# Kernel tuning notes

Hardware: AMD Instinct MI355X
Metric: run time of the kernel (lower is better)

## Reference

```python
import jax, jax.numpy as jnp
import numpy as np

N_NODES = 50000
N_EDGES = 800000
IN_DIM = 256
HID_DIM = 512
OUT_DIM = 256


def setup_inputs() -> dict:
    key = jax.random.key(0)
    ks = jax.random.split(key, 8)
    x = jax.random.normal(ks[0], (N_NODES, IN_DIM), dtype=jnp.float32)
    src = jax.random.randint(ks[1], (N_EDGES,), 0, N_NODES, dtype=jnp.int32)
    dst = jax.random.randint(ks[2], (N_EDGES,), 0, N_NODES, dtype=jnp.int32)
    s = 1.0 / np.sqrt(IN_DIM)
    W_self = jax.random.uniform(ks[3], (IN_DIM, HID_DIM), jnp.float32, -s, s)
    W_neigh = jax.random.uniform(ks[4], (IN_DIM, HID_DIM), jnp.float32, -s, s)
    b_enc = jnp.zeros((HID_DIM,), jnp.float32)
    s2 = 1.0 / np.sqrt(HID_DIM)
    W_dec = jax.random.uniform(ks[5], (HID_DIM, OUT_DIM), jnp.float32, -s2, s2)
    b_dec = jax.random.uniform(ks[6], (OUT_DIM,), jnp.float32, -s2, s2)
    return {"x": x, "src": src, "dst": dst, "W_self": W_self,
            "W_neigh": W_neigh, "b_enc": b_enc, "W_dec": W_dec, "b_dec": b_dec}


def reference(x, src, dst, W_self, W_neigh, b_enc, W_dec, b_dec):
    n = x.shape[0]
    # mean neighbor aggregation: scatter-sum src features onto dst, divide by in-degree
    deg = jax.ops.segment_sum(jnp.ones(dst.shape, x.dtype), dst, num_segments=n)
    neigh_sum = jax.ops.segment_sum(x[src], dst, num_segments=n)  # [N, in_dim]
    neigh_mean = neigh_sum / jnp.clip(deg, 1.0)[:, None]
    # SAGEConv 'mean': fc_self(x) + fc_neigh(h_neigh) + bias, then relu
    h = jax.nn.relu(x @ W_self + neigh_mean @ W_neigh + b_enc)  # [N, hid]
    reconstructed = h @ W_dec + b_dec  # [N, out]
    return (reconstructed, h)
```

## Files before the change

### kernel.cpp

```cpp
#include <hip/hip_runtime.h>
#include <stdint.h>

#define N_NODES 50000
#define N_EDGES 800000
#define IN_DIM 256
#define HID_DIM 512
#define OUT_DIM 256
#define SCAN_BLOCKS 196

__device__ __forceinline__ uint16_t f2b(float f) {
    uint32_t u = __builtin_bit_cast(uint32_t, f);
    uint32_t r = (u + 0x7fffu + ((u >> 16) & 1u)) >> 16;
    return (uint16_t)r;
}
__device__ __forceinline__ float b2f(uint16_t h) {
    uint32_t u = ((uint32_t)h) << 16;
    return __builtin_bit_cast(float, u);
}

__device__ __forceinline__ void async_copy16(const void* g, void* l) {
    __builtin_amdgcn_global_load_lds(
        (const __attribute__((address_space(1))) uint32_t*)g,
        (__attribute__((address_space(3))) uint32_t*)l,
        16, 0, 0);
}

typedef __bf16 bf16x8 __attribute__((ext_vector_type(8)));
typedef float f32x4 __attribute__((ext_vector_type(4)));

#if __has_builtin(__builtin_amdgcn_cvt_pk_fp8_f32) && __has_builtin(__builtin_amdgcn_cvt_pk_f32_fp8)
#define HW_FP8 1
#endif

__device__ __forceinline__ uint8_t enc_e4m3_sw(float f) {
    uint32_t u = __builtin_bit_cast(uint32_t, f);
    uint32_t s = (u >> 24) & 0x80u;
    float a = fabsf(f);
    if (!(a > 0.f)) return (uint8_t)s;
    if (a >= 448.f) return (uint8_t)(s | 0x7E);
    int ebits = (int)((u >> 23) & 255u) - 127;
    if (ebits < -6) {
        int q = (int)rintf(a * 512.0f);
        if (q <= 0) return (uint8_t)s;
        if (q < 8)  return (uint8_t)(s | (uint32_t)q);
        return (uint8_t)(s | 0x08u);
    }
    float scale = exp2f((float)(3 - ebits));
    int q = (int)rintf(a * scale);
    if (q == 16) { ebits++; q = 8; }
    return (uint8_t)(s | (uint32_t)((ebits + 7) << 3) | (uint32_t)(q - 8));
}
__device__ __forceinline__ float dec_e4m3_sw(uint32_t b) {
    uint32_t sgn = b >> 7, e = (b >> 3) & 15u, m = b & 7u;
    float v;
    if (e) v = __builtin_bit_cast(float, ((e + 120u) << 23) | (m << 20));
    else   v = (float)m * 0.001953125f;
    return sgn ? -v : v;
}

__device__ __forceinline__ uint32_t pack4_fp8(float4 v) {
#ifdef HW_FP8
    int w = 0;
    w = __builtin_amdgcn_cvt_pk_fp8_f32(v.x, v.y, w, false);
    w = __builtin_amdgcn_cvt_pk_fp8_f32(v.z, v.w, w, true);
    return (uint32_t)w;
#else
    return (uint32_t)enc_e4m3_sw(v.x) | ((uint32_t)enc_e4m3_sw(v.y) << 8) |
           ((uint32_t)enc_e4m3_sw(v.z) << 16) | ((uint32_t)enc_e4m3_sw(v.w) << 24);
#endif
}
__device__ __forceinline__ void unpack4_fp8(uint32_t w, float f[4]) {
#ifdef HW_FP8
    auto lo = __builtin_amdgcn_cvt_pk_f32_fp8((int)w, false);
    auto hi = __builtin_amdgcn_cvt_pk_f32_fp8((int)w, true);
    f[0] = lo[0]; f[1] = lo[1]; f[2] = hi[0]; f[3] = hi[1];
#else
    f[0] = dec_e4m3_sw(w & 255u); f[1] = dec_e4m3_sw((w >> 8) & 255u);
    f[2] = dec_e4m3_sw((w >> 16) & 255u); f[3] = dec_e4m3_sw(w >> 24);
#endif
}

__global__ void k_prep(const float* __restrict__ x, uint16_t* __restrict__ A,
                       uint32_t* __restrict__ Xq,
                       const float* __restrict__ Ws, const float* __restrict__ Wn,
                       const float* __restrict__ Wd,
                       uint16_t* __restrict__ Wc, uint16_t* __restrict__ Wt,
                       uint32_t* __restrict__ deg) {
    int b = blockIdx.x, t = threadIdx.x;
    if (b < 12500) {
        int id = b * 256 + t;
        int row = id >> 6, q = id & 63;
        float4 v = ((const float4*)x)[id];
        ushort4 o;
        o.x = f2b(v.x); o.y = f2b(v.y); o.z = f2b(v.z); o.w = f2b(v.w);
        *(ushort4*)(A + (size_t)row * 512 + q * 4) = o;
        Xq[id] = pack4_fp8(v);
    } else if (b < 12696) {
        int i = (b - 12500) * 256 + t;
        if (i < N_NODES) deg[i] = 0u;
    } else if (b < 13720) {
        int id = (b - 12696) * 256 + t;
        int n = id >> 9, k = id & 511;
        float v = (k < 256) ? Ws[(size_t)k * 512 + n] : Wn[(size_t)(k - 256) * 512 + n];
        Wc[(size_t)n * 512 + k] = f2b(v);
    } else {
        int id = (b - 13720) * 256 + t;
        int n = id >> 9, k = id & 511;
        Wt[(size_t)n * 512 + k] = f2b(Wd[(size_t)k * 256 + n]);
    }
}

__global__ void k_deg(const int* __restrict__ dst, uint32_t* __restrict__ deg) {
    int e = blockIdx.x * 256 + threadIdx.x;
    if (e < N_EDGES) atomicAdd(&deg[dst[e]], 1u);
}

__global__ void k_scan1(const uint32_t* __restrict__ deg, uint32_t* __restrict__ psum) {
    __shared__ uint32_t wsum[4];
    int b = blockIdx.x, t = threadIdx.x;
    int i = b * 256 + t;
    int v = (i < N_NODES) ? (int)deg[i] : 0;
#pragma unroll
    for (int o = 1; o < 64; o <<= 1) v += __shfl_xor(v, o);
    if ((t & 63) == 0) wsum[t >> 6] = (uint32_t)v;
    __syncthreads();
    if (t == 0) psum[b] = wsum[0] + wsum[1] + wsum[2] + wsum[3];
}

__global__ void k_scan2(const uint32_t* __restrict__ psum, uint32_t* __restrict__ pbase,
                        uint32_t* __restrict__ off) {
    __shared__ uint32_t sb[256];
    int t = threadIdx.x;
    uint32_t v = (t < SCAN_BLOCKS) ? psum[t] : 0u;
    sb[t] = v;
    __syncthreads();
#pragma unroll
    for (int o = 1; o < 256; o <<= 1) {
        uint32_t u = (t >= o) ? sb[t - o] : 0u;
        __syncthreads();
        sb[t] += u;
        __syncthreads();
    }
    if (t < SCAN_BLOCKS) pbase[t] = sb[t] - v;
    if (t == 0) off[N_NODES] = N_EDGES;
}

__global__ void k_scan3(const uint32_t* __restrict__ deg, const uint32_t* __restrict__ pbase,
                        uint32_t* __restrict__ off, uint32_t* __restrict__ cur) {
    __shared__ uint32_t sb[256];
    int b = blockIdx.x, t = threadIdx.x;
    int i = b * 256 + t;
    uint32_t v = (i < N_NODES) ? deg[i] : 0u;
    sb[t] = v;
    __syncthreads();
#pragma unroll
    for (int o = 1; o < 256; o <<= 1) {
        uint32_t u = (t >= o) ? sb[t - o] : 0u;
        __syncthreads();
        sb[t] += u;
        __syncthreads();
    }
    if (i < N_NODES) {
        uint32_t e = pbase[b] + sb[t] - v;
        off[i] = e;
        cur[i] = e;
    }
}

__global__ void k_scatter(const int* __restrict__ src, const int* __restrict__ dst,
                          uint32_t* __restrict__ cur, int* __restrict__ esrc) {
    int e = blockIdx.x * 256 + threadIdx.x;
    if (e >= N_EDGES) return;
    int d = dst[e];
    uint32_t pos = atomicAdd(&cur[d], 1u);
    esrc[pos] = src[e];
}

__global__ __launch_bounds__(256) void k_agg(const uint32_t* __restrict__ off,
                                             const int* __restrict__ esrc,
                                             const uint32_t* __restrict__ Xq,
                                             uint16_t* __restrict__ A) {
    int node = blockIdx.x * 4 + (threadIdx.x >> 6);
    if (node >= N_NODES) return;
    int lane = threadIdx.x & 63;
    const uint32_t* Xl = Xq + lane;
    uint32_t s0 = off[node], s1 = off[node + 1];
    float a0 = 0.f, a1 = 0.f, a2 = 0.f, a3 = 0.f;
    uint32_t j = s0;
    for (; j + 8 <= s1; j += 8) {
        int s_[8];
#pragma unroll
        for (int t = 0; t < 8; ++t) s_[t] = esrc[j + t];
        uint32_t w_[8];
#pragma unroll
        for (int t = 0; t < 8; ++t) w_[t] = Xl[(size_t)s_[t] * 64];
#pragma unroll
        for (int t = 0; t < 8; ++t) {
            float f[4];
            unpack4_fp8(w_[t], f);
            a0 += f[0]; a1 += f[1]; a2 += f[2]; a3 += f[3];
        }
    }
    if (j + 4 <= s1) {
        int s_[4];
#pragma unroll
        for (int t = 0; t < 4; ++t) s_[t] = esrc[j + t];
        uint32_t w_[4];
#pragma unroll
        for (int t = 0; t < 4; ++t) w_[t] = Xl[(size_t)s_[t] * 64];
#pragma unroll
        for (int t = 0; t < 4; ++t) {
            float f[4];
            unpack4_fp8(w_[t], f);
            a0 += f[0]; a1 += f[1]; a2 += f[2]; a3 += f[3];
        }
        j += 4;
    }
    for (; j < s1; ++j) {
        uint32_t w0 = Xl[(size_t)esrc[j] * 64];
        float f[4];
        unpack4_fp8(w0, f);
        a0 += f[0]; a1 += f[1]; a2 += f[2]; a3 += f[3];
    }
    float inv = 1.0f / (float)max(s1 - s0, 1u);
    ushort4 o;
    o.x = f2b(a0 * inv); o.y = f2b(a1 * inv); o.z = f2b(a2 * inv); o.w = f2b(a3 * inv);
    *(ushort4*)(A + (size_t)node * 512 + 256 + lane * 4) = o;
}

template <int N, int NY, bool RELU, bool WBF16>
__global__ __launch_bounds__(256, 2) void k_gemm(const uint16_t* __restrict__ A,
                                                 const uint16_t* __restrict__ Bt,
                                                 const float* __restrict__ bias,
                                                 float* __restrict__ Cf,
                                                 uint16_t* __restrict__ Cb, int M) {
    constexpr int K = 512;
    constexpr int BK = 64;
    __shared__ __align__(1024) uint16_t As[128 * BK];
    __shared__ __align__(1024) uint16_t Bs[128 * BK];
    const int tid = threadIdx.x;
    const int wave = tid >> 6, lane = tid & 63;
    const int wm = wave >> 1, wn = wave & 1;

    const int nwg = gridDim.x;
    const int bid = blockIdx.x;
    const int xcd = bid & 7, o = bid >> 3;
    const int q = nwg >> 3, r = nwg & 7;
    const int work = (xcd < r ? xcd * (q + 1) : r * (q + 1) + (xcd - r) * q) + o;
    const int m0 = (work / NY) * 128;
    const int n0 = (work % NY) * 128;

    const int l15 = lane & 15, l4 = lane >> 4;

    f32x4 acc[4][4] = {};

    for (int k0 = 0; k0 < K; k0 += BK) {
        __syncthreads();
#pragma unroll
        for (int j = 0; j < 4; ++j) {
            int c = j * 256 + tid;
            int row = c >> 3, p = c & 7;
            int s = p ^ (row & 7);
            int grA = min(m0 + row, M - 1);
            async_copy16(A + (size_t)grA * 512 + k0 + s * 8,
                         (char*)As + j * 4096 + wave * 1024);
            int grB = n0 + row;
            async_copy16(Bt + (size_t)grB * 512 + k0 + s * 8,
                         (char*)Bs + j * 4096 + wave * 1024);
        }
        __syncthreads();
#pragma unroll
        for (int kk = 0; kk < 2; ++kk) {
            bf16x8 af[4], bfr[4];
#pragma unroll
            for (int m = 0; m < 4; ++m) {
                int row = wm * 64 + m * 16 + l15;
                int s = (kk * 4 + l4) ^ (row & 7);
                af[m] = *(const bf16x8*)((const char*)As + row * 128 + s * 16);
            }
#pragma unroll
            for (int n = 0; n < 4; ++n) {
                int row = wn * 64 + n * 16 + l15;
                int s = (kk * 4 + l4) ^ (row & 7);
                bfr[n] = *(const bf16x8*)((const char*)Bs + row * 128 + s * 16);
            }
#pragma unroll
            for (int m = 0; m < 4; ++m)
#pragma unroll
                for (int n = 0; n < 4; ++n)
                    acc[m][n] = __builtin_amdgcn_mfma_f32_16x16x32_bf16(
                        af[m], bfr[n], acc[m][n], 0, 0, 0);
        }
    }

#pragma unroll
    for (int m = 0; m < 4; ++m) {
        int rbase = m0 + wm * 64 + m * 16 + l4 * 4;
#pragma unroll
        for (int i = 0; i < 4; ++i) {
            int r2 = rbase + i;
            if (r2 < M) {
#pragma unroll
                for (int n = 0; n < 4; ++n) {
                    int cidx = n0 + wn * 64 + n * 16 + l15;
                    float v = acc[m][n][i] + bias[cidx];
                    if (RELU) v = fmaxf(v, 0.f);
                    Cf[(size_t)r2 * N + cidx] = v;
                    if constexpr (WBF16) Cb[(size_t)r2 * N + cidx] = f2b(v);
                }
            }
        }
    }
}

extern "C" void kernel_launch(void* const* d_in, const int* in_sizes, int n_in,
                              void* d_out, int out_size, void* d_ws, size_t ws_size,
                              hipStream_t stream) {
    const float* x     = (const float*)d_in[0];
    const int*   src   = (const int*)d_in[1];
    const int*   dst   = (const int*)d_in[2];
    const float* Wself = (const float*)d_in[3];
    const float* Wneigh= (const float*)d_in[4];
    const float* benc  = (const float*)d_in[5];
    const float* Wdec  = (const float*)d_in[6];
    const float* bdec  = (const float*)d_in[7];

    float* out_recon = (float*)d_out;
    float* out_h     = (float*)d_out + (size_t)N_NODES * OUT_DIM;

    char* ws = (char*)d_ws;
    uint16_t* A    = (uint16_t*)(ws);
    uint16_t* Hb   = (uint16_t*)(ws + 51200000);
    uint16_t* Wc   = (uint16_t*)(ws + 102400000);
    uint16_t* Wd   = (uint16_t*)(ws + 102924288);
    uint32_t* deg  = (uint32_t*)(ws + 103186432);
    uint32_t* off  = (uint32_t*)(ws + 103386432);
    uint32_t* cur  = (uint32_t*)(ws + 103586560);
    int*     esrc  = (int*)(ws + 103786560);
    uint32_t* psum = (uint32_t*)(ws + 106986560);
    uint32_t* pbase= (uint32_t*)(ws + 106987344);
    uint32_t* Xq   = (uint32_t*)(ws + 106988544);

    k_prep<<<14232, 256, 0, stream>>>(x, A, Xq, Wself, Wneigh, Wdec, Wc, Wd, deg);
    k_deg<<<3125, 256, 0, stream>>>(dst, deg);
    k_scan1<<<SCAN_BLOCKS, 256, 0, stream>>>(deg, psum);
    k_scan2<<<1, 256, 0, stream>>>(psum, pbase, off);
    k_scan3<<<SCAN_BLOCKS, 256, 0, stream>>>(deg, pbase, off, cur);
    k_scatter<<<3125, 256, 0, stream>>>(src, dst, cur, esrc);
    k_agg<<<12500, 256, 0, stream>>>(off, esrc, Xq, A);
    k_gemm<512, 4, true, true><<<1564, 256, 0, stream>>>(A, Wc, benc, out_h, Hb, N_NODES);
    k_gemm<256, 2, false, false><<<782, 256, 0, stream>>>(Hb, Wd, bdec, out_recon, nullptr, N_NODES);
}
```

Baseline: 226.5 us.

## Drop bf16 H copy; decoder reads fp32 H and converts in-kernel; merge scan kernels

The encoder GEMM no longer writes a separate bf16 copy of h. The decoder GEMM now loads the fp32 h output directly and converts it to bf16 while staging it into LDS. This removes a 51 MB write, but the decoder must read twice the bytes with synchronous loads instead of async LDS copies. Separately, the two scan phases are fused: each block computes its own base by reducing the preceding partial sums, which removes one kernel launch.

```diff
diff --git a/kernel.cpp b/kernel.cpp
--- a/kernel.cpp
+++ b/kernel.cpp
@@ -127,32 +127,20 @@
     if (t == 0) psum[b] = wsum[0] + wsum[1] + wsum[2] + wsum[3];
 }
 
-__global__ void k_scan2(const uint32_t* __restrict__ psum, uint32_t* __restrict__ pbase,
-                        uint32_t* __restrict__ off) {
+__global__ void k_scan23(const uint32_t* __restrict__ deg, const uint32_t* __restrict__ psum,
+                         uint32_t* __restrict__ off, uint32_t* __restrict__ cur) {
     __shared__ uint32_t sb[256];
-    int t = threadIdx.x;
-    uint32_t v = (t < SCAN_BLOCKS) ? psum[t] : 0u;
-    sb[t] = v;
-    __syncthreads();
-#pragma unroll
-    for (int o = 1; o < 256; o <<= 1) {
-        uint32_t u = (t >= o) ? sb[t - o] : 0u;
-        __syncthreads();
-        sb[t] += u;
-        __syncthreads();
-    }
-    if (t < SCAN_BLOCKS) pbase[t] = sb[t] - v;
-    if (t == 0) off[N_NODES] = N_EDGES;
-}
-
-__global__ void k_scan3(const uint32_t* __restrict__ deg, const uint32_t* __restrict__ pbase,
-                        uint32_t* __restrict__ off, uint32_t* __restrict__ cur) {
-    __shared__ uint32_t sb[256];
+    __shared__ uint32_t wsum[4];
     int b = blockIdx.x, t = threadIdx.x;
     int i = b * 256 + t;
+    uint32_t pv = (t < b) ? psum[t] : 0u;
+#pragma unroll
+    for (int o = 1; o < 64; o <<= 1) pv += __shfl_xor(pv, o);
+    if ((t & 63) == 0) wsum[t >> 6] = pv;
     uint32_t v = (i < N_NODES) ? deg[i] : 0u;
     sb[t] = v;
     __syncthreads();
+    uint32_t base = wsum[0] + wsum[1] + wsum[2] + wsum[3];
 #pragma unroll
     for (int o = 1; o < 256; o <<= 1) {
         uint32_t u = (t >= o) ? sb[t - o] : 0u;
@@ -161,10 +149,11 @@
         __syncthreads();
     }
     if (i < N_NODES) {
-        uint32_t e = pbase[b] + sb[t] - v;
+        uint32_t e = base + sb[t] - v;
         off[i] = e;
         cur[i] = e;
     }
+    if (b == 0 && t == 0) off[N_NODES] = N_EDGES;
 }
 
 __global__ void k_scatter(const int* __restrict__ src, const int* __restrict__ dst,
@@ -228,12 +217,11 @@
     *(ushort4*)(A + (size_t)node * 512 + 256 + lane * 4) = o;
 }
 
-template <int N, int NY, bool RELU, bool WBF16>
-__global__ __launch_bounds__(256, 2) void k_gemm(const uint16_t* __restrict__ A,
-                                                 const uint16_t* __restrict__ Bt,
-                                                 const float* __restrict__ bias,
-                                                 float* __restrict__ Cf,
-                                                 uint16_t* __restrict__ Cb, int M) {
+template <int N, int NY, bool RELU>
+__global__ __launch_bounds__(256, 2) void k_gemm_enc(const uint16_t* __restrict__ A,
+                                                     const uint16_t* __restrict__ Bt,
+                                                     const float* __restrict__ bias,
+                                                     float* __restrict__ Cf, int M) {
     constexpr int K = 512;
     constexpr int BK = 64;
     __shared__ __align__(1024) uint16_t As[128 * BK];
@@ -306,7 +294,98 @@
                     float v = acc[m][n][i] + bias[cidx];
                     if (RELU) v = fmaxf(v, 0.f);
                     Cf[(size_t)r2 * N + cidx] = v;
-                    if constexpr (WBF16) Cb[(size_t)r2 * N + cidx] = f2b(v);
+                }
+            }
+        }
+    }
+}
+
+template <int N, int NY>
+__global__ __launch_bounds__(256, 2) void k_gemm_dec(const float* __restrict__ Af,
+                                                     const uint16_t* __restrict__ Bt,
+                                                     const float* __restrict__ bias,
+                                                     float* __restrict__ Cf, int M) {
+    constexpr int K = 512;
+    constexpr int BK = 64;
+    __shared__ __align__(1024) uint16_t As[128 * BK];
+    __shared__ __align__(1024) uint16_t Bs[128 * BK];
+    const int tid = threadIdx.x;
+    const int wave = tid >> 6, lane = tid & 63;
+    const int wm = wave >> 1, wn = wave & 1;
+
+    const int nwg = gridDim.x;
+    const int bid = blockIdx.x;
+    const int xcd = bid & 7, o = bid >> 3;
+    const int q = nwg >> 3, r = nwg & 7;
+    const int work = (xcd < r ? xcd * (q + 1) : r * (q + 1) + (xcd - r) * q) + o;
+    const int m0 = (work / NY) * 128;
+    const int n0 = (work % NY) * 128;
+
+    const int l15 = lane & 15, l4 = lane >> 4;
+
+    f32x4 acc[4][4] = {};
+
+    for (int k0 = 0; k0 < K; k0 += BK) {
+        __syncthreads();
+#pragma unroll
+        for (int j = 0; j < 4; ++j) {
+            int c = j * 256 + tid;
+            int row = c >> 3, p = c & 7;
+            int grB = n0 + row;
+            async_copy16(Bt + (size_t)grB * 512 + k0 + (p ^ (row & 7)) * 8,
+                         (char*)Bs + j * 4096 + wave * 1024);
+        }
+#pragma unroll
+        for (int j = 0; j < 4; ++j) {
+            int c = j * 256 + tid;
+            int row = c >> 3, p = c & 7;
+            int grA = min(m0 + row, M - 1);
+            const float* srcp = Af + (size_t)grA * 512 + k0 + p * 8;
+            float4 v0 = *(const float4*)(srcp);
+            float4 v1 = *(const float4*)(srcp + 4);
+            uint32_t d0 = (uint32_t)f2b(v0.x) | ((uint32_t)f2b(v0.y) << 16);
+            uint32_t d1 = (uint32_t)f2b(v0.z) | ((uint32_t)f2b(v0.w) << 16);
+            uint32_t d2 = (uint32_t)f2b(v1.x) | ((uint32_t)f2b(v1.y) << 16);
+            uint32_t d3 = (uint32_t)f2b(v1.z) | ((uint32_t)f2b(v1.w) << 16);
+            *(uint4*)((char*)As + row * 128 + (p ^ (row & 7)) * 16) =
+                make_uint4(d0, d1, d2, d3);
+        }
+        __syncthreads();
+#pragma unroll
+        for (int kk = 0; kk < 2; ++kk) {
+            bf16x8 af[4], bfr[4];
+#pragma unroll
+            for (int m = 0; m < 4; ++m) {
+                int row = wm * 64 + m * 16 + l15;
+                int s = (kk * 4 + l4) ^ (row & 7);
+                af[m] = *(const bf16x8*)((const char*)As + row * 128 + s * 16);
+            }
+#pragma unroll
+            for (int n = 0; n < 4; ++n) {
+                int row = wn * 64 + n * 16 + l15;
+                int s = (kk * 4 + l4) ^ (row & 7);
+                bfr[n] = *(const bf16x8*)((const char*)Bs + row * 128 + s * 16);
+            }
+#pragma unroll
+            for (int m = 0; m < 4; ++m)
+#pragma unroll
+                for (int n = 0; n < 4; ++n)
+                    acc[m][n] = __builtin_amdgcn_mfma_f32_16x16x32_bf16(
+                        af[m], bfr[n], acc[m][n], 0, 0, 0);
+        }
+    }
+
+#pragma unroll
+    for (int m = 0; m < 4; ++m) {
+        int rbase = m0 + wm * 64 + m * 16 + l4 * 4;
+#pragma unroll
+        for (int i = 0; i < 4; ++i) {
+            int r2 = rbase + i;
+            if (r2 < M) {
+#pragma unroll
+                for (int n = 0; n < 4; ++n) {
+                    int cidx = n0 + wn * 64 + n * 16 + l15;
+                    Cf[(size_t)r2 * N + cidx] = acc[m][n][i] + bias[cidx];
                 }
             }
         }
@@ -330,24 +409,21 @@
 
     char* ws = (char*)d_ws;
     uint16_t* A    = (uint16_t*)(ws);
-    uint16_t* Hb   = (uint16_t*)(ws + 51200000);
-    uint16_t* Wc   = (uint16_t*)(ws + 102400000);
-    uint16_t* Wd   = (uint16_t*)(ws + 102924288);
-    uint32_t* deg  = (uint32_t*)(ws + 103186432);
-    uint32_t* off  = (uint32_t*)(ws + 103386432);
-    uint32_t* cur  = (uint32_t*)(ws + 103586560);
-    int*     esrc  = (int*)(ws + 103786560);
-    uint32_t* psum = (uint32_t*)(ws + 106986560);
-    uint32_t* pbase= (uint32_t*)(ws + 106987344);
-    uint32_t* Xq   = (uint32_t*)(ws + 106988544);
+    uint16_t* Wc   = (uint16_t*)(ws + 51200000);
+    uint16_t* Wd   = (uint16_t*)(ws + 51724288);
+    uint32_t* deg  = (uint32_t*)(ws + 51986432);
+    uint32_t* off  = (uint32_t*)(ws + 52186432);
+    uint32_t* cur  = (uint32_t*)(ws + 52386560);
+    int*     esrc  = (int*)(ws + 52586560);
+    uint32_t* psum = (uint32_t*)(ws + 55786560);
+    uint32_t* Xq   = (uint32_t*)(ws + 55788544);
 
     k_prep<<<14232, 256, 0, stream>>>(x, A, Xq, Wself, Wneigh, Wdec, Wc, Wd, deg);
     k_deg<<<3125, 256, 0, stream>>>(dst, deg);
     k_scan1<<<SCAN_BLOCKS, 256, 0, stream>>>(deg, psum);
-    k_scan2<<<1, 256, 0, stream>>>(psum, pbase, off);
-    k_scan3<<<SCAN_BLOCKS, 256, 0, stream>>>(deg, pbase, off, cur);
+    k_scan23<<<SCAN_BLOCKS, 256, 0, stream>>>(deg, psum, off, cur);
     k_scatter<<<3125, 256, 0, stream>>>(src, dst, cur, esrc);
     k_agg<<<12500, 256, 0, stream>>>(off, esrc, Xq, A);
-    k_gemm<512, 4, true, true><<<1564, 256, 0, stream>>>(A, Wc, benc, out_h, Hb, N_NODES);
-    k_gemm<256, 2, false, false><<<782, 256, 0, stream>>>(Hb, Wd, bdec, out_recon, nullptr, N_NODES);
-}
+    k_gemm_enc<512, 4, true><<<1564, 256, 0, stream>>>(A, Wc, benc, out_h, N_NODES);
+    k_gemm_dec<256, 2><<<782, 256, 0, stream>>>(out_h, Wd, bdec, out_recon, N_NODES);
+}
```

New measurement: 219.7 us. 3.0% less time.
